# Optimization experiments

Measured on AMD Instinct MI355X. Metric: run time of the kernel, lower is better.

Reference implementation:

```python
import jax, jax.numpy as jnp
import numpy as np


def setup_inputs() -> dict:
    key = jax.random.key(0)
    k1, k2, k3, k4 = jax.random.split(key, 4)
    B, S, d_in, d_out = 4, 2048, 1024, 1024
    scale = 1.0 / np.sqrt(d_in)
    x = jax.random.normal(k1, (B, S, d_in), dtype=jnp.float32)
    # Linear weights stored as [d_in, d_out] so projection is x @ W
    Wq = jax.random.normal(k2, (d_in, d_out), dtype=jnp.float32) * scale
    Wk = jax.random.normal(k3, (d_in, d_out), dtype=jnp.float32) * scale
    Wv = jax.random.normal(k4, (d_in, d_out), dtype=jnp.float32) * scale
    return {"x": x, "Wq": Wq, "Wk": Wk, "Wv": Wv}


def reference(x, Wq, Wk, Wv):
    # QKV projections (no bias, matching qkv_bias=False)
    q = jnp.einsum("bsi,io->bso", x, Wq)
    k = jnp.einsum("bsi,io->bso", x, Wk)
    v = jnp.einsum("bsi,io->bso", x, Wv)
    d_k = k.shape[-1]
    # attn_scores = q @ k^T, causal mask (strict upper triangle -> -inf)
    scores = jnp.einsum("bqd,bkd->bqk", q, k)
    S = scores.shape[-1]
    causal = jnp.tril(jnp.ones((S, S), dtype=bool))  # True where allowed
    scores = jnp.where(causal, scores, -jnp.inf)
    attn = jax.nn.softmax(scores / jnp.sqrt(jnp.asarray(d_k, scores.dtype)), axis=-1)
    # dropout p=0.0 -> identity
    return jnp.einsum("bqk,bkd->bqd", attn, v)
```

## Files before the change

### kernel.cpp

```cpp
#include <hip/hip_runtime.h>

typedef _Float16 half8 __attribute__((ext_vector_type(8)));
typedef _Float16 half4 __attribute__((ext_vector_type(4)));
typedef float f32x4 __attribute__((ext_vector_type(4)));

#define ATT_SCALE 0.03125f
#define S_LEN 2048
#define D_DIM 1024
#define NB 4

__device__ __forceinline__ void async_cp16(const _Float16* g, _Float16* l)
{
    __builtin_amdgcn_global_load_lds(
        (const __attribute__((address_space(1))) void*)g,
        (__attribute__((address_space(3))) void*)l, 16, 0, 0);
}

__device__ __forceinline__ void gemm_core64(const _Float16* __restrict__ Ag,
                                            const _Float16* __restrict__ Bg,
                                            int lda, int ldb, int ksteps64,
                                            f32x4 acc[4][4])
{
    __shared__ _Float16 As[128 * 64];
    __shared__ _Float16 Bs[128 * 64];

    const int t    = threadIdx.x;
    const int wave = t >> 6;
    const int lane = t & 63;
    const int wm   = (wave >> 1) * 64;
    const int wn   = (wave & 1) * 64;
    const int lg   = lane >> 4;
    const int lr   = lane & 15;

    const int tr = t >> 3;
    const int tc = ((t & 7) ^ (tr & 7)) * 8;
    const int ldso = wave * 512;

    const _Float16* ap0 = Ag + (long)(0 * 32 + tr) * lda + tc;
    const _Float16* ap1 = Ag + (long)(1 * 32 + tr) * lda + tc;
    const _Float16* ap2 = Ag + (long)(2 * 32 + tr) * lda + tc;
    const _Float16* ap3 = Ag + (long)(3 * 32 + tr) * lda + tc;
    const _Float16* bp0 = Bg + (long)(0 * 32 + tr) * ldb + tc;
    const _Float16* bp1 = Bg + (long)(1 * 32 + tr) * ldb + tc;
    const _Float16* bp2 = Bg + (long)(2 * 32 + tr) * ldb + tc;
    const _Float16* bp3 = Bg + (long)(3 * 32 + tr) * ldb + tc;

    const int arow = wm + lr;
    const int brow = wn + lr;

    for (int ks = 0; ks < ksteps64; ++ks) {
        __syncthreads();
        async_cp16(ap0, As + 0 * 2048 + ldso);
        async_cp16(ap1, As + 1 * 2048 + ldso);
        async_cp16(ap2, As + 2 * 2048 + ldso);
        async_cp16(ap3, As + 3 * 2048 + ldso);
        async_cp16(bp0, Bs + 0 * 2048 + ldso);
        async_cp16(bp1, Bs + 1 * 2048 + ldso);
        async_cp16(bp2, Bs + 2 * 2048 + ldso);
        async_cp16(bp3, Bs + 3 * 2048 + ldso);
        __syncthreads();

        ap0 += 64; ap1 += 64; ap2 += 64; ap3 += 64;
        bp0 += 64; bp1 += 64; bp2 += 64; bp3 += 64;

#pragma unroll
        for (int kk = 0; kk < 2; ++kk) {
            half8 af[4], bf[4];
#pragma unroll
            for (int mf = 0; mf < 4; ++mf) {
                const int row = arow + mf * 16;
                const int hof = (kk * 32 + lg * 8) ^ ((row & 7) * 8);
                af[mf] = *(const half8*)&As[row * 64 + hof];
            }
#pragma unroll
            for (int nf = 0; nf < 4; ++nf) {
                const int row = brow + nf * 16;
                const int hof = (kk * 32 + lg * 8) ^ ((row & 7) * 8);
                bf[nf] = *(const half8*)&Bs[row * 64 + hof];
            }
#pragma unroll
            for (int mf = 0; mf < 4; ++mf)
#pragma unroll
                for (int nf = 0; nf < 4; ++nf)
                    acc[mf][nf] = __builtin_amdgcn_mfma_f32_16x16x32_f16(
                        af[mf], bf[nf], acc[mf][nf], 0, 0, 0);
        }
    }
}

__global__ void init_kernel(const float* __restrict__ X, _Float16* __restrict__ Xh,
                            float4* __restrict__ out, float* __restrict__ rs)
{
    const int i = blockIdx.x * 256 + threadIdx.x;
    float4 v = ((const float4*)X)[i];
    half4 h;
    h.x = (_Float16)v.x; h.y = (_Float16)v.y; h.z = (_Float16)v.z; h.w = (_Float16)v.w;
    ((half4*)Xh)[i] = h;
    out[i] = (float4){0.f, 0.f, 0.f, 0.f};
    if (i < NB * S_LEN) rs[i] = 0.f;
}

__global__ void transpose_w_kernel(const float* __restrict__ Wq,
                                   const float* __restrict__ Wk,
                                   const float* __restrict__ Wv,
                                   _Float16* __restrict__ Wt)
{
    __shared__ float tile[32][33];
    const int n0 = blockIdx.x * 32, k0 = blockIdx.y * 32, w = blockIdx.z;
    const float* Wsrc = (w == 0) ? Wq : (w == 1) ? Wk : Wv;
    _Float16* dst = Wt + (long)w * D_DIM * D_DIM;
    const int tx = threadIdx.x, ty = threadIdx.y;
#pragma unroll
    for (int j = 0; j < 4; ++j)
        tile[ty + 8 * j][tx] = Wsrc[(long)(k0 + ty + 8 * j) * D_DIM + n0 + tx];
    __syncthreads();
#pragma unroll
    for (int j = 0; j < 4; ++j)
        dst[(long)(n0 + ty + 8 * j) * D_DIM + k0 + tx] = (_Float16)tile[tx][ty + 8 * j];
}

__global__ __launch_bounds__(256) void proj_kernel(const _Float16* __restrict__ Xh,
                                                   const _Float16* __restrict__ Wt,
                                                   _Float16* __restrict__ Q,
                                                   _Float16* __restrict__ K,
                                                   _Float16* __restrict__ V)
{
    const int flat = blockIdx.x;
    const int swz  = (flat & 7) * 192 + (flat >> 3);
    const int nt = swz & 7, mt = (swz >> 3) & 63, w = swz >> 9;

    f32x4 acc[4][4];
#pragma unroll
    for (int i = 0; i < 4; ++i)
#pragma unroll
        for (int j = 0; j < 4; ++j) acc[i][j] = (f32x4){0.f, 0.f, 0.f, 0.f};

    const _Float16* Ag = Xh + (long)mt * 128 * D_DIM;
    const _Float16* Bg = Wt + (long)w * D_DIM * D_DIM + (long)nt * 128 * D_DIM;
    gemm_core64(Ag, Bg, D_DIM, D_DIM, D_DIM / 64, acc);

    _Float16* C = (w == 0) ? Q : (w == 1) ? K : V;
    const int t = threadIdx.x, wave = t >> 6, lane = t & 63;
    const int wm = (wave >> 1) * 64, wn = (wave & 1) * 64;
    const int lg = lane >> 4, lr = lane & 15;
    const long row0 = (long)mt * 128 + wm + 4 * lg;
    const long col0 = (long)nt * 128 + wn + lr;
#pragma unroll
    for (int i = 0; i < 4; ++i)
#pragma unroll
        for (int j = 0; j < 4; ++j)
#pragma unroll
            for (int r = 0; r < 4; ++r)
                C[(row0 + i * 16 + r) * D_DIM + col0 + j * 16] = (_Float16)acc[i][j][r];
}

__global__ __launch_bounds__(256) void transpose_v_kernel(const _Float16* __restrict__ V,
                                                          _Float16* __restrict__ Vt)
{
    __shared__ _Float16 tile[64][72];
    const int d0 = blockIdx.x * 64, s0 = blockIdx.y * 64;
    const long b = blockIdx.z;
    const _Float16* Vb = V + b * S_LEN * D_DIM;
    _Float16* Vtb = Vt + b * D_DIM * S_LEN;
    const int t = threadIdx.x;
    const int sr = t >> 3, c8 = (t & 7) * 8;

    *(half8*)&tile[sr][c8]      = *(const half8*)&Vb[(long)(s0 + sr) * D_DIM + d0 + c8];
    *(half8*)&tile[sr + 32][c8] = *(const half8*)&Vb[(long)(s0 + sr + 32) * D_DIM + d0 + c8];
    __syncthreads();

    const int dr = t >> 3, s8 = (t & 7) * 8;
    half8 o0, o1;
#pragma unroll
    for (int e = 0; e < 8; ++e) {
        o0[e] = tile[s8 + e][dr];
        o1[e] = tile[s8 + e][dr + 32];
    }
    *(half8*)&Vtb[(long)(d0 + dr) * S_LEN + s0 + s8]      = o0;
    *(half8*)&Vtb[(long)(d0 + dr + 32) * S_LEN + s0 + s8] = o1;
}

__global__ __launch_bounds__(256) void scores_exp_kernel(const _Float16* __restrict__ Q,
                                                         const _Float16* __restrict__ K,
                                                         _Float16* __restrict__ P,
                                                         float* __restrict__ row_sum)
{
    const int xcd = blockIdx.x & 7;
    const int idx = blockIdx.x >> 3;
    const int b   = idx / 17;
    const int l   = idx % 17;
    int qt, kt;
    if (l <= xcd) { qt = xcd;      kt = l; }
    else          { qt = 15 - xcd; kt = l - xcd - 1; }

    f32x4 acc[4][4];
#pragma unroll
    for (int i = 0; i < 4; ++i)
#pragma unroll
        for (int j = 0; j < 4; ++j) acc[i][j] = (f32x4){0.f, 0.f, 0.f, 0.f};

    const _Float16* Ag = Q + ((long)b * S_LEN + qt * 128) * D_DIM;
    const _Float16* Bg = K + ((long)b * S_LEN + kt * 128) * D_DIM;
    gemm_core64(Ag, Bg, D_DIM, D_DIM, D_DIM / 64, acc);

    _Float16* Pb = P + (long)b * S_LEN * S_LEN;
    float* rsb = row_sum + (long)b * S_LEN;
    const int t = threadIdx.x, wave = t >> 6, lane = t & 63;
    const int wm = (wave >> 1) * 64, wn = (wave & 1) * 64;
    const int lg = lane >> 4, lr = lane & 15;
    const int row0 = qt * 128 + wm + 4 * lg;
    const int col0 = kt * 128 + wn + lr;

#pragma unroll
    for (int i = 0; i < 4; ++i) {
#pragma unroll
        for (int r = 0; r < 4; ++r) {
            const int row = row0 + i * 16 + r;
            float s = 0.f;
#pragma unroll
            for (int j = 0; j < 4; ++j) {
                const int col = col0 + j * 16;
                float p = (col <= row) ? __expf(acc[i][j][r] * ATT_SCALE) : 0.f;
                s += p;
                Pb[(long)row * S_LEN + col] = (_Float16)p;
            }
#pragma unroll
            for (int off = 1; off < 16; off <<= 1) s += __shfl_xor(s, off, 64);
            if (lr == 0) atomicAdd(&rsb[row], s);
        }
    }
}

__global__ __launch_bounds__(256) void pv_kernel(const _Float16* __restrict__ P,
                                                 const _Float16* __restrict__ Vt,
                                                 const float* __restrict__ row_sum,
                                                 float* __restrict__ O)
{
    const int xcd = blockIdx.x & 7;
    int r = blockIdx.x >> 3;
    const int b = r / 24;  r %= 24;
    const int j = r >> 3;
    const int nt = r & 7;
    const int sl = (j == 0) ? (7 - xcd) : (j == 1 ? 8 + 2 * xcd : 9 + 2 * xcd);

    int qt, k0, ks64;
    if (sl < 8) { qt = sl; k0 = 0; ks64 = (qt + 1) * 2; }
    else {
        const int e = sl - 8;
        qt = 8 + (e >> 1);
        ks64 = qt + 1;
        k0 = (e & 1) * ks64 * 64;
    }

    f32x4 acc[4][4];
#pragma unroll
    for (int i = 0; i < 4; ++i)
#pragma unroll
        for (int jj = 0; jj < 4; ++jj) acc[i][jj] = (f32x4){0.f, 0.f, 0.f, 0.f};

    const _Float16* Ag = P + ((long)b * S_LEN + qt * 128) * S_LEN + k0;
    const _Float16* Bg = Vt + (long)b * D_DIM * S_LEN + (long)nt * 128 * S_LEN + k0;
    gemm_core64(Ag, Bg, S_LEN, S_LEN, ks64, acc);

    float* Ob = O + (long)b * S_LEN * D_DIM;
    const float* rsb = row_sum + (long)b * S_LEN;
    const int t = threadIdx.x, wave = t >> 6, lane = t & 63;
    const int wm = (wave >> 1) * 64, wn = (wave & 1) * 64;
    const int lg = lane >> 4, lr = lane & 15;
    const long row0 = qt * 128 + wm + 4 * lg;
    const long col0 = (long)nt * 128 + wn + lr;

    if (sl < 8) {
#pragma unroll
        for (int i = 0; i < 4; ++i)
#pragma unroll
            for (int rr = 0; rr < 4; ++rr) {
                const float inv = 1.f / rsb[row0 + i * 16 + rr];
#pragma unroll
                for (int jj = 0; jj < 4; ++jj)
                    Ob[(row0 + i * 16 + rr) * D_DIM + col0 + jj * 16] = acc[i][jj][rr] * inv;
            }
    } else {
#pragma unroll
        for (int i = 0; i < 4; ++i)
#pragma unroll
            for (int rr = 0; rr < 4; ++rr) {
                const float inv = 1.f / rsb[row0 + i * 16 + rr];
#pragma unroll
                for (int jj = 0; jj < 4; ++jj)
                    atomicAdd(&Ob[(row0 + i * 16 + rr) * D_DIM + col0 + jj * 16],
                              acc[i][jj][rr] * inv);
            }
    }
}

extern "C" void kernel_launch(void* const* d_in, const int* in_sizes, int n_in,
                              void* d_out, int out_size, void* d_ws, size_t ws_size,
                              hipStream_t stream)
{
    const float* x  = (const float*)d_in[0];
    const float* Wq = (const float*)d_in[1];
    const float* Wk = (const float*)d_in[2];
    const float* Wv = (const float*)d_in[3];
    float* out = (float*)d_out;

    char* ws = (char*)d_ws;
    const long MiB = 1024 * 1024;
    _Float16* Q  = (_Float16*)(ws + 0 * MiB);
    _Float16* K  = (_Float16*)(ws + 16 * MiB);
    _Float16* V  = (_Float16*)(ws + 32 * MiB);
    _Float16* Vt = (_Float16*)(ws + 48 * MiB);
    _Float16* Xh = (_Float16*)(ws + 64 * MiB);
    _Float16* Wt = (_Float16*)(ws + 80 * MiB);
    _Float16* P  = (_Float16*)(ws + 86 * MiB);
    float*    RS = (float*)   (ws + 118 * MiB);

    init_kernel<<<dim3(8192), dim3(256), 0, stream>>>(x, Xh, (float4*)out, RS);
    transpose_w_kernel<<<dim3(32, 32, 3), dim3(32, 8), 0, stream>>>(Wq, Wk, Wv, Wt);
    proj_kernel<<<dim3(1536), dim3(256), 0, stream>>>(Xh, Wt, Q, K, V);
    transpose_v_kernel<<<dim3(16, 32, 4), dim3(256), 0, stream>>>(V, Vt);
    scores_exp_kernel<<<dim3(544), dim3(256), 0, stream>>>(Q, K, P, RS);
    pv_kernel<<<dim3(768), dim3(256), 0, stream>>>(P, Vt, RS, out);
}
```

Baseline: 174.9 us.

## Fuse QKV projections into one block sharing X tiles; merge weight transpose into init

The projection kernel now computes the Q, K and V tiles for one 128x128 output block together. It loads each X tile once and reuses it across all three weight matrices, using a 32-wide K step and 48 accumulators per thread. The weight transpose is folded into the init kernel as extra blocks, which removes one launch. The grid drops from 1536 to 512 blocks, so fewer blocks may be resident and register pressure rises. The k-loop also has no double buffering, which could expose load latency.

```diff
diff --git a/kernel.cpp b/kernel.cpp
--- a/kernel.cpp
+++ b/kernel.cpp
@@ -89,27 +89,30 @@
 }
 
 __global__ void init_kernel(const float* __restrict__ X, _Float16* __restrict__ Xh,
-                            float4* __restrict__ out, float* __restrict__ rs)
-{
-    const int i = blockIdx.x * 256 + threadIdx.x;
-    float4 v = ((const float4*)X)[i];
-    half4 h;
-    h.x = (_Float16)v.x; h.y = (_Float16)v.y; h.z = (_Float16)v.z; h.w = (_Float16)v.w;
-    ((half4*)Xh)[i] = h;
-    out[i] = (float4){0.f, 0.f, 0.f, 0.f};
-    if (i < NB * S_LEN) rs[i] = 0.f;
-}
-
-__global__ void transpose_w_kernel(const float* __restrict__ Wq,
-                                   const float* __restrict__ Wk,
-                                   const float* __restrict__ Wv,
-                                   _Float16* __restrict__ Wt)
-{
+                            float4* __restrict__ out, float* __restrict__ rs,
+                            const float* __restrict__ Wq, const float* __restrict__ Wk,
+                            const float* __restrict__ Wv, _Float16* __restrict__ Wt)
+{
+    const int bid = blockIdx.x;
+    const int t   = threadIdx.x;
+    if (bid < 8192) {
+        const int i = bid * 256 + t;
+        float4 v = ((const float4*)X)[i];
+        half4 h;
+        h.x = (_Float16)v.x; h.y = (_Float16)v.y; h.z = (_Float16)v.z; h.w = (_Float16)v.w;
+        ((half4*)Xh)[i] = h;
+        out[i] = (float4){0.f, 0.f, 0.f, 0.f};
+        if (i < NB * S_LEN) rs[i] = 0.f;
+        return;
+    }
     __shared__ float tile[32][33];
-    const int n0 = blockIdx.x * 32, k0 = blockIdx.y * 32, w = blockIdx.z;
+    const int bb = bid - 8192;
+    const int w  = bb >> 10;
+    const int rem = bb & 1023;
+    const int n0 = (rem & 31) * 32, k0 = (rem >> 5) * 32;
     const float* Wsrc = (w == 0) ? Wq : (w == 1) ? Wk : Wv;
     _Float16* dst = Wt + (long)w * D_DIM * D_DIM;
-    const int tx = threadIdx.x, ty = threadIdx.y;
+    const int tx = t & 31, ty = t >> 5;
 #pragma unroll
     for (int j = 0; j < 4; ++j)
         tile[ty + 8 * j][tx] = Wsrc[(long)(k0 + ty + 8 * j) * D_DIM + n0 + tx];
@@ -125,33 +128,95 @@
                                                    _Float16* __restrict__ K,
                                                    _Float16* __restrict__ V)
 {
-    const int flat = blockIdx.x;
-    const int swz  = (flat & 7) * 192 + (flat >> 3);
-    const int nt = swz & 7, mt = (swz >> 3) & 63, w = swz >> 9;
-
-    f32x4 acc[4][4];
-#pragma unroll
-    for (int i = 0; i < 4; ++i)
-#pragma unroll
-        for (int j = 0; j < 4; ++j) acc[i][j] = (f32x4){0.f, 0.f, 0.f, 0.f};
-
-    const _Float16* Ag = Xh + (long)mt * 128 * D_DIM;
-    const _Float16* Bg = Wt + (long)w * D_DIM * D_DIM + (long)nt * 128 * D_DIM;
-    gemm_core64(Ag, Bg, D_DIM, D_DIM, D_DIM / 64, acc);
-
-    _Float16* C = (w == 0) ? Q : (w == 1) ? K : V;
-    const int t = threadIdx.x, wave = t >> 6, lane = t & 63;
-    const int wm = (wave >> 1) * 64, wn = (wave & 1) * 64;
-    const int lg = lane >> 4, lr = lane & 15;
+    __shared__ _Float16 As[128 * 32];
+    __shared__ _Float16 Bs[3][128 * 32];
+
+    const int bid = blockIdx.x;
+    const int g   = (bid & 7) * 64 + (bid >> 3);
+    const int mt  = g >> 3;
+    const int nt  = g & 7;
+
+    const int t    = threadIdx.x;
+    const int wave = t >> 6;
+    const int lane = t & 63;
+    const int wm   = (wave >> 1) * 64;
+    const int wn   = (wave & 1) * 64;
+    const int lg   = lane >> 4;
+    const int lr   = lane & 15;
+
+    const int sr  = t >> 2;
+    const int scg = ((t & 3) ^ (sr & 3)) * 8;
+    const int ldso = wave * 512;
+
+    const _Float16* a0 = Xh + ((long)mt * 128 + sr) * D_DIM + scg;
+    const _Float16* a1 = a0 + 64 * D_DIM;
+    const _Float16* b0[3], * b1[3];
+#pragma unroll
+    for (int w = 0; w < 3; ++w) {
+        b0[w] = Wt + (long)w * D_DIM * D_DIM + ((long)nt * 128 + sr) * D_DIM + scg;
+        b1[w] = b0[w] + 64 * D_DIM;
+    }
+
+    f32x4 acc[3][4][4];
+#pragma unroll
+    for (int w = 0; w < 3; ++w)
+#pragma unroll
+        for (int i = 0; i < 4; ++i)
+#pragma unroll
+            for (int j = 0; j < 4; ++j) acc[w][i][j] = (f32x4){0.f, 0.f, 0.f, 0.f};
+
+    const int arow = wm + lr;
+    const int brow = wn + lr;
+    const int hswz = lg ^ (lr & 3);
+
+    for (int ks = 0; ks < 32; ++ks) {
+        __syncthreads();
+        async_cp16(a0, As + 0 * 2048 + ldso);
+        async_cp16(a1, As + 1 * 2048 + ldso);
+#pragma unroll
+        for (int w = 0; w < 3; ++w) {
+            async_cp16(b0[w], Bs[w] + 0 * 2048 + ldso);
+            async_cp16(b1[w], Bs[w] + 1 * 2048 + ldso);
+        }
+        __syncthreads();
+
+        a0 += 32; a1 += 32;
+#pragma unroll
+        for (int w = 0; w < 3; ++w) { b0[w] += 32; b1[w] += 32; }
+
+        half8 af[4];
+#pragma unroll
+        for (int mf = 0; mf < 4; ++mf)
+            af[mf] = *(const half8*)&As[(arow + mf * 16) * 32 + hswz * 8];
+
+#pragma unroll
+        for (int w = 0; w < 3; ++w) {
+            half8 bf[4];
+#pragma unroll
+            for (int nf = 0; nf < 4; ++nf)
+                bf[nf] = *(const half8*)&Bs[w][(brow + nf * 16) * 32 + hswz * 8];
+#pragma unroll
+            for (int mf = 0; mf < 4; ++mf)
+#pragma unroll
+                for (int nf = 0; nf < 4; ++nf)
+                    acc[w][mf][nf] = __builtin_amdgcn_mfma_f32_16x16x32_f16(
+                        af[mf], bf[nf], acc[w][mf][nf], 0, 0, 0);
+        }
+    }
+
     const long row0 = (long)mt * 128 + wm + 4 * lg;
     const long col0 = (long)nt * 128 + wn + lr;
 #pragma unroll
-    for (int i = 0; i < 4; ++i)
-#pragma unroll
-        for (int j = 0; j < 4; ++j)
-#pragma unroll
-            for (int r = 0; r < 4; ++r)
-                C[(row0 + i * 16 + r) * D_DIM + col0 + j * 16] = (_Float16)acc[i][j][r];
+    for (int w = 0; w < 3; ++w) {
+        _Float16* C = (w == 0) ? Q : (w == 1) ? K : V;
+#pragma unroll
+        for (int i = 0; i < 4; ++i)
+#pragma unroll
+            for (int j = 0; j < 4; ++j)
+#pragma unroll
+                for (int r = 0; r < 4; ++r)
+                    C[(row0 + i * 16 + r) * D_DIM + col0 + j * 16] = (_Float16)acc[w][i][j][r];
+    }
 }
 
 __global__ __launch_bounds__(256) void transpose_v_kernel(const _Float16* __restrict__ V,
@@ -315,9 +380,9 @@
     _Float16* P  = (_Float16*)(ws + 86 * MiB);
     float*    RS = (float*)   (ws + 118 * MiB);
 
-    init_kernel<<<dim3(8192), dim3(256), 0, stream>>>(x, Xh, (float4*)out, RS);
-    transpose_w_kernel<<<dim3(32, 32, 3), dim3(32, 8), 0, stream>>>(Wq, Wk, Wv, Wt);
-    proj_kernel<<<dim3(1536), dim3(256), 0, stream>>>(Xh, Wt, Q, K, V);
+    init_kernel<<<dim3(8192 + 3072), dim3(256), 0, stream>>>(x, Xh, (float4*)out, RS,
+                                                             Wq, Wk, Wv, Wt);
+    proj_kernel<<<dim3(512), dim3(256), 0, stream>>>(Xh, Wt, Q, K, V);
     transpose_v_kernel<<<dim3(16, 32, 4), dim3(256), 0, stream>>>(V, Vt);
     scores_exp_kernel<<<dim3(544), dim3(256), 0, stream>>>(Q, K, P, RS);
     pv_kernel<<<dim3(768), dim3(256), 0, stream>>>(P, Vt, RS, out);
```

Result: slower. 204.2 us (+16.7%).

## Merge prep launches, fold V transpose into scores, drop PV split-K atomics

Applied to the files above, without the earlier changes.

Folds the weight-transpose work into the init kernel and the V transpose into the scores kernel as extra blocks, cutting the launch count from six to four. The PV kernel stops splitting the K dimension for late query tiles, so each block covers the full causal range and writes the output with plain stores. That removes both the atomic adds and the zero-fill of the output. The cost is less balanced work in PV (512 blocks of very different lengths, longest first) and transpose blocks sharing the scores kernel. A no-op `*0.f` term was also added inside the exp argument.

```diff
diff --git a/kernel.cpp b/kernel.cpp
--- a/kernel.cpp
+++ b/kernel.cpp
@@ -89,27 +89,29 @@
 }
 
 __global__ void init_kernel(const float* __restrict__ X, _Float16* __restrict__ Xh,
-                            float4* __restrict__ out, float* __restrict__ rs)
-{
-    const int i = blockIdx.x * 256 + threadIdx.x;
-    float4 v = ((const float4*)X)[i];
-    half4 h;
-    h.x = (_Float16)v.x; h.y = (_Float16)v.y; h.z = (_Float16)v.z; h.w = (_Float16)v.w;
-    ((half4*)Xh)[i] = h;
-    out[i] = (float4){0.f, 0.f, 0.f, 0.f};
-    if (i < NB * S_LEN) rs[i] = 0.f;
-}
-
-__global__ void transpose_w_kernel(const float* __restrict__ Wq,
-                                   const float* __restrict__ Wk,
-                                   const float* __restrict__ Wv,
-                                   _Float16* __restrict__ Wt)
-{
+                            float* __restrict__ rs,
+                            const float* __restrict__ Wq, const float* __restrict__ Wk,
+                            const float* __restrict__ Wv, _Float16* __restrict__ Wt)
+{
+    const int bid = blockIdx.x;
+    const int t   = threadIdx.x;
+    if (bid < 8192) {
+        const int i = bid * 256 + t;
+        float4 v = ((const float4*)X)[i];
+        half4 h;
+        h.x = (_Float16)v.x; h.y = (_Float16)v.y; h.z = (_Float16)v.z; h.w = (_Float16)v.w;
+        ((half4*)Xh)[i] = h;
+        if (i < NB * S_LEN) rs[i] = 0.f;
+        return;
+    }
     __shared__ float tile[32][33];
-    const int n0 = blockIdx.x * 32, k0 = blockIdx.y * 32, w = blockIdx.z;
+    const int bb = bid - 8192;
+    const int w  = bb >> 10;
+    const int rem = bb & 1023;
+    const int n0 = (rem & 31) * 32, k0 = (rem >> 5) * 32;
     const float* Wsrc = (w == 0) ? Wq : (w == 1) ? Wk : Wv;
     _Float16* dst = Wt + (long)w * D_DIM * D_DIM;
-    const int tx = threadIdx.x, ty = threadIdx.y;
+    const int tx = t & 31, ty = t >> 5;
 #pragma unroll
     for (int j = 0; j < 4; ++j)
         tile[ty + 8 * j][tx] = Wsrc[(long)(k0 + ty + 8 * j) * D_DIM + n0 + tx];
@@ -154,37 +156,40 @@
                 C[(row0 + i * 16 + r) * D_DIM + col0 + j * 16] = (_Float16)acc[i][j][r];
 }
 
-__global__ __launch_bounds__(256) void transpose_v_kernel(const _Float16* __restrict__ V,
-                                                          _Float16* __restrict__ Vt)
-{
-    __shared__ _Float16 tile[64][72];
-    const int d0 = blockIdx.x * 64, s0 = blockIdx.y * 64;
-    const long b = blockIdx.z;
-    const _Float16* Vb = V + b * S_LEN * D_DIM;
-    _Float16* Vtb = Vt + b * D_DIM * S_LEN;
-    const int t = threadIdx.x;
-    const int sr = t >> 3, c8 = (t & 7) * 8;
-
-    *(half8*)&tile[sr][c8]      = *(const half8*)&Vb[(long)(s0 + sr) * D_DIM + d0 + c8];
-    *(half8*)&tile[sr + 32][c8] = *(const half8*)&Vb[(long)(s0 + sr + 32) * D_DIM + d0 + c8];
-    __syncthreads();
-
-    const int dr = t >> 3, s8 = (t & 7) * 8;
-    half8 o0, o1;
-#pragma unroll
-    for (int e = 0; e < 8; ++e) {
-        o0[e] = tile[s8 + e][dr];
-        o1[e] = tile[s8 + e][dr + 32];
+__global__ __launch_bounds__(256) void scores_tv_kernel(const _Float16* __restrict__ Q,
+                                                        const _Float16* __restrict__ K,
+                                                        const _Float16* __restrict__ V,
+                                                        _Float16* __restrict__ P,
+                                                        float* __restrict__ row_sum,
+                                                        _Float16* __restrict__ Vt)
+{
+    __shared__ _Float16 ttile[64][72];
+    if (blockIdx.x >= 544) {
+        const int tv = blockIdx.x - 544;
+        const int d0 = (tv & 15) * 64;
+        const int s0 = ((tv >> 4) & 31) * 64;
+        const long b = tv >> 9;
+        const _Float16* Vb = V + b * S_LEN * D_DIM;
+        _Float16* Vtb = Vt + b * D_DIM * S_LEN;
+        const int t = threadIdx.x;
+        const int sr = t >> 3, c8 = (t & 7) * 8;
+
+        *(half8*)&ttile[sr][c8]      = *(const half8*)&Vb[(long)(s0 + sr) * D_DIM + d0 + c8];
+        *(half8*)&ttile[sr + 32][c8] = *(const half8*)&Vb[(long)(s0 + sr + 32) * D_DIM + d0 + c8];
+        __syncthreads();
+
+        const int dr = t >> 3, s8 = (t & 7) * 8;
+        half8 o0, o1;
+#pragma unroll
+        for (int e = 0; e < 8; ++e) {
+            o0[e] = ttile[s8 + e][dr];
+            o1[e] = ttile[s8 + e][dr + 32];
+        }
+        *(half8*)&Vtb[(long)(d0 + dr) * S_LEN + s0 + s8]      = o0;
+        *(half8*)&Vtb[(long)(d0 + dr + 32) * S_LEN + s0 + s8] = o1;
+        return;
     }
-    *(half8*)&Vtb[(long)(d0 + dr) * S_LEN + s0 + s8]      = o0;
-    *(half8*)&Vtb[(long)(d0 + dr + 32) * S_LEN + s0 + s8] = o1;
-}
-
-__global__ __launch_bounds__(256) void scores_exp_kernel(const _Float16* __restrict__ Q,
-                                                         const _Float16* __restrict__ K,
-                                                         _Float16* __restrict__ P,
-                                                         float* __restrict__ row_sum)
-{
+
     const int xcd = blockIdx.x & 7;
     const int idx = blockIdx.x >> 3;
     const int b   = idx / 17;
@@ -220,7 +225,7 @@
 #pragma unroll
             for (int j = 0; j < 4; ++j) {
                 const int col = col0 + j * 16;
-                float p = (col <= row) ? __expf(acc[i][j][r] * ATT_SCALE) : 0.f;
+                float p = (col <= row) ? __expf(acc[i][r * 0 + j][r] * 0.f + acc[i][j][r] * ATT_SCALE) : 0.f;
                 s += p;
                 Pb[(long)row * S_LEN + col] = (_Float16)p;
             }
@@ -236,21 +241,13 @@
                                                  const float* __restrict__ row_sum,
                                                  float* __restrict__ O)
 {
-    const int xcd = blockIdx.x & 7;
-    int r = blockIdx.x >> 3;
-    const int b = r / 24;  r %= 24;
-    const int j = r >> 3;
-    const int nt = r & 7;
-    const int sl = (j == 0) ? (7 - xcd) : (j == 1 ? 8 + 2 * xcd : 9 + 2 * xcd);
-
-    int qt, k0, ks64;
-    if (sl < 8) { qt = sl; k0 = 0; ks64 = (qt + 1) * 2; }
-    else {
-        const int e = sl - 8;
-        qt = 8 + (e >> 1);
-        ks64 = qt + 1;
-        k0 = (e & 1) * ks64 * 64;
-    }
+    const int idx = blockIdx.x;
+    const int qt  = 15 - (idx >> 5);
+    const int rem = idx & 31;
+    const int nt  = rem >> 2;
+    const int b   = rem & 3;
+
+    const int ks64 = (qt + 1) * 2;
 
     f32x4 acc[4][4];
 #pragma unroll
@@ -258,8 +255,8 @@
 #pragma unroll
         for (int jj = 0; jj < 4; ++jj) acc[i][jj] = (f32x4){0.f, 0.f, 0.f, 0.f};
 
-    const _Float16* Ag = P + ((long)b * S_LEN + qt * 128) * S_LEN + k0;
-    const _Float16* Bg = Vt + (long)b * D_DIM * S_LEN + (long)nt * 128 * S_LEN + k0;
+    const _Float16* Ag = P + ((long)b * S_LEN + qt * 128) * S_LEN;
+    const _Float16* Bg = Vt + (long)b * D_DIM * S_LEN + (long)nt * 128 * S_LEN;
     gemm_core64(Ag, Bg, S_LEN, S_LEN, ks64, acc);
 
     float* Ob = O + (long)b * S_LEN * D_DIM;
@@ -270,28 +267,15 @@
     const long row0 = qt * 128 + wm + 4 * lg;
     const long col0 = (long)nt * 128 + wn + lr;
 
-    if (sl < 8) {
-#pragma unroll
-        for (int i = 0; i < 4; ++i)
-#pragma unroll
-            for (int rr = 0; rr < 4; ++rr) {
-                const float inv = 1.f / rsb[row0 + i * 16 + rr];
-#pragma unroll
-                for (int jj = 0; jj < 4; ++jj)
-                    Ob[(row0 + i * 16 + rr) * D_DIM + col0 + jj * 16] = acc[i][jj][rr] * inv;
-            }
-    } else {
-#pragma unroll
-        for (int i = 0; i < 4; ++i)
-#pragma unroll
-            for (int rr = 0; rr < 4; ++rr) {
-                const float inv = 1.f / rsb[row0 + i * 16 + rr];
-#pragma unroll
-                for (int jj = 0; jj < 4; ++jj)
-                    atomicAdd(&Ob[(row0 + i * 16 + rr) * D_DIM + col0 + jj * 16],
-                              acc[i][jj][rr] * inv);
-            }
-    }
+#pragma unroll
+    for (int i = 0; i < 4; ++i)
+#pragma unroll
+        for (int rr = 0; rr < 4; ++rr) {
+            const float inv = 1.f / rsb[row0 + i * 16 + rr];
+#pragma unroll
+            for (int jj = 0; jj < 4; ++jj)
+                Ob[(row0 + i * 16 + rr) * D_DIM + col0 + jj * 16] = acc[i][jj][rr] * inv;
+        }
 }
 
 extern "C" void kernel_launch(void* const* d_in, const int* in_sizes, int n_in,
@@ -315,10 +299,8 @@
     _Float16* P  = (_Float16*)(ws + 86 * MiB);
     float*    RS = (float*)   (ws + 118 * MiB);
 
-    init_kernel<<<dim3(8192), dim3(256), 0, stream>>>(x, Xh, (float4*)out, RS);
-    transpose_w_kernel<<<dim3(32, 32, 3), dim3(32, 8), 0, stream>>>(Wq, Wk, Wv, Wt);
+    init_kernel<<<dim3(8192 + 3072), dim3(256), 0, stream>>>(x, Xh, RS, Wq, Wk, Wv, Wt);
     proj_kernel<<<dim3(1536), dim3(256), 0, stream>>>(Xh, Wt, Q, K, V);
-    transpose_v_kernel<<<dim3(16, 32, 4), dim3(256), 0, stream>>>(V, Vt);
-    scores_exp_kernel<<<dim3(544), dim3(256), 0, stream>>>(Q, K, P, RS);
-    pv_kernel<<<dim3(768), dim3(256), 0, stream>>>(P, Vt, RS, out);
-}
+    scores_tv_kernel<<<dim3(2592), dim3(256), 0, stream>>>(Q, K, V, P, RS, Vt);
+    pv_kernel<<<dim3(512), dim3(256), 0, stream>>>(P, Vt, RS, out);
+}
```

New measurement: 155.1 us. 1.13x faster.
